# Kernel optimization log

Hardware: AMD Instinct MI355X
Metric: run time of the kernel (lower is better)

Reference implementation:

```python
import jax, jax.numpy as jnp
from jax import lax
import numpy as np

B, T, I, H, L, C = 64, 512, 128, 256, 2, 3


def _lstm_layer(x, W_ih, W_hh, b_ih, b_hh):
    # x: [B, T, in_dim]; W_ih: [4H, in_dim]; W_hh: [4H, H]
    # PyTorch gate order: i, f, g, o
    gates_x = jnp.einsum('bti,gi->btg', x, W_ih) + b_ih + b_hh  # [B, T, 4H]
    h0 = jnp.zeros((x.shape[0], W_hh.shape[1]), x.dtype)
    c0 = h0

    def step(carry, gx):
        h, c = carry
        g = gx + h @ W_hh.T  # [B, 4H]
        i, f, gg, o = jnp.split(g, 4, axis=-1)
        i = jax.nn.sigmoid(i)
        f = jax.nn.sigmoid(f)
        gg = jnp.tanh(gg)
        o = jax.nn.sigmoid(o)
        c = f * c + i * gg
        h = o * jnp.tanh(c)
        return (h, c), h

    _, hs = lax.scan(step, (h0, c0), jnp.swapaxes(gates_x, 0, 1))  # [T, B, H]
    return jnp.swapaxes(hs, 0, 1)  # [B, T, H]


def setup_inputs() -> dict:
    key = jax.random.key(0)
    ks = jax.random.split(key, 12)
    s = 1.0 / np.sqrt(H)
    u = lambda k, shape: jax.random.uniform(k, shape, jnp.float32, -s, s)
    return {
        'x': jax.random.normal(ks[0], (B, T, I), jnp.float32),
        'W_ih_0': u(ks[1], (4 * H, I)),
        'W_hh_0': u(ks[2], (4 * H, H)),
        'b_ih_0': u(ks[3], (4 * H,)),
        'b_hh_0': u(ks[4], (4 * H,)),
        'W_ih_1': u(ks[5], (4 * H, H)),
        'W_hh_1': u(ks[6], (4 * H, H)),
        'b_ih_1': u(ks[7], (4 * H,)),
        'b_hh_1': u(ks[8], (4 * H,)),
        'fc_w': u(ks[9], (C, H)),
        'fc_b': u(ks[10], (C,)),
    }


def reference(x, W_ih_0, W_hh_0, b_ih_0, b_hh_0, W_ih_1, W_hh_1, b_ih_1, b_hh_1, fc_w, fc_b):
    h = _lstm_layer(x, W_ih_0, W_hh_0, b_ih_0, b_hh_0)
    h = _lstm_layer(h, W_ih_1, W_hh_1, b_ih_1, b_hh_1)
    last = h[:, -1, :]                      # [B, H]
    logits = last @ fc_w.T + fc_b           # [B, C]
    return jax.nn.softmax(logits, axis=1)
```

## Files before the change

### kernel.cpp

```cpp
#include <hip/hip_runtime.h>
#include <cstdint>
#include <cstddef>

typedef _Float16 half2_t __attribute__((ext_vector_type(2)));
typedef _Float16 half8_t __attribute__((ext_vector_type(8)));
typedef float f32x4 __attribute__((ext_vector_type(4)));

static __device__ __forceinline__ float fdot2(half2_t a, half2_t b, float c) {
    return __builtin_amdgcn_fdot2(a, b, c, false);
}
static __device__ __forceinline__ half2_t h2(unsigned int u) {
    return __builtin_bit_cast(half2_t, u);
}
static __device__ __forceinline__ float sigm(float x) {
    return 1.f / (1.f + __expf(-x));
}
static __device__ __forceinline__ float tanh_fast(float x) {
    float ax = fabsf(x);
    float e = __expf(2.f * ax);
    float r = 1.f - 2.f / (e + 1.f);
    return copysignf(r, x);
}

__global__ __launch_bounds__(256) void prep_whh(const float* __restrict__ Whh,
                                                const float* __restrict__ bih,
                                                const float* __restrict__ bhh,
                                                uint4* __restrict__ Wp,
                                                float* __restrict__ bias) {
    int n = blockIdx.x * 256 + threadIdx.x;
    if (n < 1024) bias[n] = bih[n] + bhh[n];
    int p = n >> 9;
    int tid = n & 511;
    int g = p >> 4, u = p & 15;
    int w = tid >> 6, l = tid & 63;
    int q = l >> 5, l31 = l & 31;
    int row = g * 256 + w * 32 + l31;
    int kb = q * 128 + u * 8;
    union { uint4 u4; _Float16 h[8]; } cv;
#pragma unroll
    for (int i = 0; i < 8; ++i) cv.h[i] = (_Float16)Whh[row * 256 + kb + i];
    Wp[p * 512 + tid] = cv.u4;
}

__global__ __launch_bounds__(256) void cvt_f16(const float* __restrict__ in,
                                               _Float16* __restrict__ out, int n4) {
    int i = blockIdx.x * 256 + threadIdx.x;
    if (i < n4) {
        float4 v = ((const float4*)in)[i];
        union { ushort4 u; _Float16 h[4]; } cv;
        cv.h[0] = (_Float16)v.x; cv.h[1] = (_Float16)v.y;
        cv.h[2] = (_Float16)v.z; cv.h[3] = (_Float16)v.w;
        ((ushort4*)out)[i] = cv.u;
    }
}

__global__ __launch_bounds__(256) void gemm_mfma(const _Float16* __restrict__ A,
                                                 const _Float16* __restrict__ Bw,
                                                 const float* __restrict__ bias,
                                                 float* __restrict__ Cmat, int K) {
    __shared__ _Float16 As[64][72];
    __shared__ _Float16 Bs[64][72];
    const int tid = threadIdx.x;
    const int wave = tid >> 6, lane = tid & 63;
    const int quad = lane >> 4, l16 = lane & 15;
    const int m0 = blockIdx.x * 64, n0 = blockIdx.y * 64;
    const int sr = tid >> 2;
    const int sc = (tid & 3) * 16;

    f32x4 acc[4] = {};

    for (int k0 = 0; k0 < K; k0 += 64) {
        const uint4 a0v = *(const uint4*)(A + (size_t)(m0 + sr) * K + k0 + sc);
        const uint4 a1v = *(const uint4*)(A + (size_t)(m0 + sr) * K + k0 + sc + 8);
        const uint4 b0v = *(const uint4*)(Bw + (size_t)(n0 + sr) * K + k0 + sc);
        const uint4 b1v = *(const uint4*)(Bw + (size_t)(n0 + sr) * K + k0 + sc + 8);
        __syncthreads();
        *(uint4*)&As[sr][sc] = a0v;
        *(uint4*)&As[sr][sc + 8] = a1v;
        *(uint4*)&Bs[sr][sc] = b0v;
        *(uint4*)&Bs[sr][sc + 8] = b1v;
        __syncthreads();
#pragma unroll
        for (int kc = 0; kc < 64; kc += 32) {
            half8_t af = *(const half8_t*)&As[wave * 16 + l16][kc + quad * 8];
#pragma unroll
            for (int nb = 0; nb < 4; ++nb) {
                half8_t bf = *(const half8_t*)&Bs[nb * 16 + l16][kc + quad * 8];
                acc[nb] = __builtin_amdgcn_mfma_f32_16x16x32_f16(af, bf, acc[nb], 0, 0, 0);
            }
        }
    }
#pragma unroll
    for (int nb = 0; nb < 4; ++nb) {
#pragma unroll
        for (int i = 0; i < 4; ++i) {
            int row = m0 + wave * 16 + quad * 4 + i;
            int col = n0 + nb * 16 + l16;
            Cmat[(size_t)row * 1024 + col] = acc[nb][i] + bias[col];
        }
    }
}

__global__ __launch_bounds__(512, 2)
void lstm_scan(const float* __restrict__ gx,
               const uint4* __restrict__ Wp,
               _Float16* __restrict__ h_out,
               int store_all) {
    const int b = blockIdx.x;
    const int tid = threadIdx.x;
    const int w = tid >> 6;
    const int l = tid & 63;
    const int q = l >> 5;
    const int l31 = l & 31;
    const int j = w * 32 + l31;

    __shared__ uint4 wlds[16 * 512];
    __shared__ _Float16 hbuf[2][256] __attribute__((aligned(16)));
    __shared__ _Float16 hist[16][256] __attribute__((aligned(16)));

#pragma unroll
    for (int p = 0; p < 16; ++p) wlds[p * 512 + tid] = Wp[(48 + p) * 512 + tid];
    uint4 wreg[48];
#pragma unroll
    for (int p = 0; p < 48; ++p) wreg[p] = Wp[p * 512 + tid];

    if (tid < 256) hbuf[0][tid] = (_Float16)0.f;
    float c = 0.f;
    const float* gxb = gx + (size_t)b * 512 * 1024 + (size_t)(q * 512 + j);
    float gA = gxb[0], gB = gxb[256];
    __syncthreads();

    for (int t = 0; t < 512; ++t) {
        float gA_n = 0.f, gB_n = 0.f;
        if (t < 511) {
            gA_n = gxb[(size_t)(t + 1) * 1024];
            gB_n = gxb[(size_t)(t + 1) * 1024 + 256];
        }

        const char* hp = (const char*)&hbuf[t & 1][0] + q * 256;
        float a0 = 0.f, a1 = 0.f, a2 = 0.f, a3 = 0.f;
#pragma unroll
        for (int u = 0; u < 16; ++u) {
            const uint4 hv = *(const uint4*)(hp + u * 16);
            const uint4 w0 = wreg[u];
            const uint4 w1 = wreg[16 + u];
            const uint4 w2 = wreg[32 + u];
            const uint4 w3 = wlds[u * 512 + tid];
            a0 = fdot2(h2(w0.x), h2(hv.x), a0);
            a1 = fdot2(h2(w1.x), h2(hv.x), a1);
            a2 = fdot2(h2(w2.x), h2(hv.x), a2);
            a3 = fdot2(h2(w3.x), h2(hv.x), a3);
            a0 = fdot2(h2(w0.y), h2(hv.y), a0);
            a1 = fdot2(h2(w1.y), h2(hv.y), a1);
            a2 = fdot2(h2(w2.y), h2(hv.y), a2);
            a3 = fdot2(h2(w3.y), h2(hv.y), a3);
            a0 = fdot2(h2(w0.z), h2(hv.z), a0);
            a1 = fdot2(h2(w1.z), h2(hv.z), a1);
            a2 = fdot2(h2(w2.z), h2(hv.z), a2);
            a3 = fdot2(h2(w3.z), h2(hv.z), a3);
            a0 = fdot2(h2(w0.w), h2(hv.w), a0);
            a1 = fdot2(h2(w1.w), h2(hv.w), a1);
            a2 = fdot2(h2(w2.w), h2(hv.w), a2);
            a3 = fdot2(h2(w3.w), h2(hv.w), a3);
        }
        if (q == 0) { a0 += gA; a1 += gB; }
        else        { a2 += gA; a3 += gB; }
        a0 += __shfl_xor(a0, 32);
        a1 += __shfl_xor(a1, 32);
        a2 += __shfl_xor(a2, 32);
        a3 += __shfl_xor(a3, 32);

        const float iv = sigm(a0);
        const float fv = sigm(a1);
        const float gv = tanh_fast(a2);
        const float ov = sigm(a3);
        c = fv * c + iv * gv;
        const _Float16 hh = (_Float16)(ov * tanh_fast(c));

        if (q == 0) hbuf[(t + 1) & 1][j] = hh;
        else if (store_all) hist[t & 15][j] = hh;
        gA = gA_n; gB = gB_n;

        asm volatile("s_waitcnt lgkmcnt(0)" ::: "memory");
        __builtin_amdgcn_s_barrier();
        asm volatile("" ::: "memory");

        if (store_all && (t & 7) == 7) {
            const int s = tid >> 6, e = tid & 63;
            const int s0 = (t - 7) & 15;
            const uint2 v = *(const uint2*)&hist[s0 + s][e * 4];
            *(uint2*)(h_out + (size_t)b * 512 * 256 +
                      (size_t)(t - 7 + s) * 256 + e * 4) = v;
        }
    }
    if (!store_all && tid < 256) {
        h_out[(size_t)b * 256 + tid] = hbuf[0][tid];
    }
}

__global__ __launch_bounds__(64) void fc_softmax(const _Float16* __restrict__ hlast,
                                                 const float* __restrict__ fcw,
                                                 const float* __restrict__ fcb,
                                                 float* __restrict__ out) {
    const int b = blockIdx.x;
    const int lane = threadIdx.x;
    const _Float16* h = hlast + (size_t)b * 256;
    float p0 = 0.f, p1 = 0.f, p2 = 0.f;
    for (int k = lane; k < 256; k += 64) {
        float hv = (float)h[k];
        p0 += hv * fcw[k];
        p1 += hv * fcw[256 + k];
        p2 += hv * fcw[512 + k];
    }
#pragma unroll
    for (int off = 32; off > 0; off >>= 1) {
        p0 += __shfl_down(p0, off);
        p1 += __shfl_down(p1, off);
        p2 += __shfl_down(p2, off);
    }
    if (lane == 0) {
        float l0 = p0 + fcb[0], l1 = p1 + fcb[1], l2 = p2 + fcb[2];
        float m = fmaxf(l0, fmaxf(l1, l2));
        float e0 = __expf(l0 - m), e1 = __expf(l1 - m), e2 = __expf(l2 - m);
        float s = 1.f / (e0 + e1 + e2);
        out[b * 3 + 0] = e0 * s;
        out[b * 3 + 1] = e1 * s;
        out[b * 3 + 2] = e2 * s;
    }
}

extern "C" void kernel_launch(void* const* d_in, const int* in_sizes, int n_in,
                              void* d_out, int out_size, void* d_ws, size_t ws_size,
                              hipStream_t stream) {
    const float* x    = (const float*)d_in[0];
    const float* Wih0 = (const float*)d_in[1];
    const float* Whh0 = (const float*)d_in[2];
    const float* bih0 = (const float*)d_in[3];
    const float* bhh0 = (const float*)d_in[4];
    const float* Wih1 = (const float*)d_in[5];
    const float* Whh1 = (const float*)d_in[6];
    const float* bih1 = (const float*)d_in[7];
    const float* bhh1 = (const float*)d_in[8];
    const float* fcw  = (const float*)d_in[9];
    const float* fcb  = (const float*)d_in[10];
    float* out = (float*)d_out;

    char* ws = (char*)d_ws;
    float* gx        = (float*)ws;     ws += (size_t)32768 * 1024 * 4;
    _Float16* h0f    = (_Float16*)ws;  ws += (size_t)32768 * 256 * 2;
    _Float16* xh     = (_Float16*)ws;  ws += (size_t)32768 * 128 * 2;
    _Float16* hlast  = (_Float16*)ws;  ws += (size_t)64 * 256 * 2;
    _Float16* Wih0h  = (_Float16*)ws;  ws += (size_t)1024 * 128 * 2;
    _Float16* Wih1h  = (_Float16*)ws;  ws += (size_t)1024 * 256 * 2;
    uint4* Wp0       = (uint4*)ws;     ws += (size_t)1024 * 256 * 2;
    uint4* Wp1       = (uint4*)ws;     ws += (size_t)1024 * 256 * 2;
    float* bias0     = (float*)ws;     ws += 4096;
    float* bias1     = (float*)ws;     ws += 4096;

    prep_whh<<<128, 256, 0, stream>>>(Whh0, bih0, bhh0, Wp0, bias0);
    prep_whh<<<128, 256, 0, stream>>>(Whh1, bih1, bhh1, Wp1, bias1);
    cvt_f16<<<4096, 256, 0, stream>>>(x, xh, 32768 * 128 / 4);
    cvt_f16<<<128, 256, 0, stream>>>(Wih0, Wih0h, 1024 * 128 / 4);
    cvt_f16<<<256, 256, 0, stream>>>(Wih1, Wih1h, 1024 * 256 / 4);

    gemm_mfma<<<dim3(512, 16), 256, 0, stream>>>(xh, Wih0h, bias0, gx, 128);
    lstm_scan<<<64, 512, 0, stream>>>(gx, Wp0, h0f, 1);

    gemm_mfma<<<dim3(512, 16), 256, 0, stream>>>(h0f, Wih1h, bias1, gx, 256);
    lstm_scan<<<64, 512, 0, stream>>>(gx, Wp1, hlast, 0);

    fc_softmax<<<64, 64, 0, stream>>>(hlast, fcw, fcb, out);
}
```

Measured before the change: 1.793 ms.

## Give each LSTM scan thread a full hidden unit with more register-resident weights

The recurrent scan drops from 512 to 256 threads per block, so each thread computes the whole K=256 dot product for one hidden unit. This removes the cross-half shuffle reductions and the duplicated gate-input loads. The packed weight layout is rebuilt so 104 uint4 chunks sit in registers and 24 in LDS, with the h and LDS weight reads software-pipelined inside the loop. The trade-off is half as many waves to hide latency, twice the serial dot-product work per thread, and very high VGPR pressure that could cause spills.

```diff
diff --git a/kernel.cpp b/kernel.cpp
--- a/kernel.cpp
+++ b/kernel.cpp
@@ -29,17 +29,15 @@
                                                 float* __restrict__ bias) {
     int n = blockIdx.x * 256 + threadIdx.x;
     if (n < 1024) bias[n] = bih[n] + bhh[n];
-    int p = n >> 9;
-    int tid = n & 511;
-    int g = p >> 4, u = p & 15;
-    int w = tid >> 6, l = tid & 63;
-    int q = l >> 5, l31 = l & 31;
-    int row = g * 256 + w * 32 + l31;
-    int kb = q * 128 + u * 8;
+    int p = n >> 8;
+    int j = n & 255;
+    int g = p >> 5, u = p & 31;
+    int row = g * 256 + j;
+    int kb = u * 8;
     union { uint4 u4; _Float16 h[8]; } cv;
 #pragma unroll
     for (int i = 0; i < 8; ++i) cv.h[i] = (_Float16)Whh[row * 256 + kb + i];
-    Wp[p * 512 + tid] = cv.u4;
+    Wp[p * 256 + j] = cv.u4;
 }
 
 __global__ __launch_bounds__(256) void cvt_f16(const float* __restrict__ in,
@@ -101,51 +99,57 @@
     }
 }
 
-__global__ __launch_bounds__(512, 2)
+__global__ __launch_bounds__(256, 1)
 void lstm_scan(const float* __restrict__ gx,
                const uint4* __restrict__ Wp,
                _Float16* __restrict__ h_out,
                int store_all) {
     const int b = blockIdx.x;
-    const int tid = threadIdx.x;
-    const int w = tid >> 6;
-    const int l = tid & 63;
-    const int q = l >> 5;
-    const int l31 = l & 31;
-    const int j = w * 32 + l31;
-
-    __shared__ uint4 wlds[16 * 512];
+    const int j = threadIdx.x;
+
+    __shared__ uint4 wlds[24 * 256];
     __shared__ _Float16 hbuf[2][256] __attribute__((aligned(16)));
     __shared__ _Float16 hist[16][256] __attribute__((aligned(16)));
 
 #pragma unroll
-    for (int p = 0; p < 16; ++p) wlds[p * 512 + tid] = Wp[(48 + p) * 512 + tid];
-    uint4 wreg[48];
-#pragma unroll
-    for (int p = 0; p < 48; ++p) wreg[p] = Wp[p * 512 + tid];
-
-    if (tid < 256) hbuf[0][tid] = (_Float16)0.f;
+    for (int p = 0; p < 24; ++p) wlds[p * 256 + j] = Wp[(104 + p) * 256 + j];
+    uint4 wreg[104];
+#pragma unroll
+    for (int p = 0; p < 104; ++p) wreg[p] = Wp[p * 256 + j];
+
+    hbuf[0][j] = (_Float16)0.f;
     float c = 0.f;
-    const float* gxb = gx + (size_t)b * 512 * 1024 + (size_t)(q * 512 + j);
-    float gA = gxb[0], gB = gxb[256];
+    _Float16 last_h = (_Float16)0.f;
+    const float* gxb = gx + (size_t)b * 512 * 1024 + j;
+    float g0 = gxb[0], g1 = gxb[256], g2 = gxb[512], g3 = gxb[768];
     __syncthreads();
 
     for (int t = 0; t < 512; ++t) {
-        float gA_n = 0.f, gB_n = 0.f;
+        float n0 = 0.f, n1 = 0.f, n2 = 0.f, n3 = 0.f;
         if (t < 511) {
-            gA_n = gxb[(size_t)(t + 1) * 1024];
-            gB_n = gxb[(size_t)(t + 1) * 1024 + 256];
-        }
-
-        const char* hp = (const char*)&hbuf[t & 1][0] + q * 256;
+            const float* gxn = gxb + (size_t)(t + 1) * 1024;
+            n0 = gxn[0]; n1 = gxn[256]; n2 = gxn[512]; n3 = gxn[768];
+        }
+
+        const uint4* hb = (const uint4*)&hbuf[t & 1][0];
+        uint4 hv0 = hb[0], hv1 = hb[1];
+        uint4 ws0 = wlds[0 * 256 + j], ws1 = wlds[1 * 256 + j];
+
         float a0 = 0.f, a1 = 0.f, a2 = 0.f, a3 = 0.f;
 #pragma unroll
-        for (int u = 0; u < 16; ++u) {
-            const uint4 hv = *(const uint4*)(hp + u * 16);
+        for (int u = 0; u < 32; ++u) {
+            const uint4 hv = (u & 1) ? hv1 : hv0;
+            if (u + 2 < 32) {
+                if (u & 1) hv1 = hb[u + 2]; else hv0 = hb[u + 2];
+            }
+            const uint4 w3 = (u < 8) ? wreg[96 + u] : ((u & 1) ? ws1 : ws0);
+            if (u >= 8 && u < 30) {
+                if (u & 1) ws1 = wlds[(u - 6) * 256 + j];
+                else       ws0 = wlds[(u - 6) * 256 + j];
+            }
             const uint4 w0 = wreg[u];
-            const uint4 w1 = wreg[16 + u];
-            const uint4 w2 = wreg[32 + u];
-            const uint4 w3 = wlds[u * 512 + tid];
+            const uint4 w1 = wreg[32 + u];
+            const uint4 w2 = wreg[64 + u];
             a0 = fdot2(h2(w0.x), h2(hv.x), a0);
             a1 = fdot2(h2(w1.x), h2(hv.x), a1);
             a2 = fdot2(h2(w2.x), h2(hv.x), a2);
@@ -163,12 +167,7 @@
             a2 = fdot2(h2(w2.w), h2(hv.w), a2);
             a3 = fdot2(h2(w3.w), h2(hv.w), a3);
         }
-        if (q == 0) { a0 += gA; a1 += gB; }
-        else        { a2 += gA; a3 += gB; }
-        a0 += __shfl_xor(a0, 32);
-        a1 += __shfl_xor(a1, 32);
-        a2 += __shfl_xor(a2, 32);
-        a3 += __shfl_xor(a3, 32);
+        a0 += g0; a1 += g1; a2 += g2; a3 += g3;
 
         const float iv = sigm(a0);
         const float fv = sigm(a1);
@@ -176,25 +175,23 @@
         const float ov = sigm(a3);
         c = fv * c + iv * gv;
         const _Float16 hh = (_Float16)(ov * tanh_fast(c));
-
-        if (q == 0) hbuf[(t + 1) & 1][j] = hh;
-        else if (store_all) hist[t & 15][j] = hh;
-        gA = gA_n; gB = gB_n;
+        hbuf[(t + 1) & 1][j] = hh;
+        last_h = hh;
+        if (store_all) hist[t & 15][j] = hh;
+        g0 = n0; g1 = n1; g2 = n2; g3 = n3;
 
         asm volatile("s_waitcnt lgkmcnt(0)" ::: "memory");
         __builtin_amdgcn_s_barrier();
         asm volatile("" ::: "memory");
 
         if (store_all && (t & 7) == 7) {
-            const int s = tid >> 6, e = tid & 63;
             const int s0 = (t - 7) & 15;
-            const uint2 v = *(const uint2*)&hist[s0 + s][e * 4];
-            *(uint2*)(h_out + (size_t)b * 512 * 256 +
-                      (size_t)(t - 7 + s) * 256 + e * 4) = v;
-        }
-    }
-    if (!store_all && tid < 256) {
-        h_out[(size_t)b * 256 + tid] = hbuf[0][tid];
+            const uint4 v = *(const uint4*)((const char*)hist + s0 * 512 + j * 16);
+            *(uint4*)(h_out + (size_t)b * 512 * 256 + (size_t)(t - 7) * 256 + j * 8) = v;
+        }
+    }
+    if (!store_all) {
+        h_out[(size_t)b * 256 + j] = last_h;
     }
 }
 
@@ -264,10 +261,10 @@
     cvt_f16<<<256, 256, 0, stream>>>(Wih1, Wih1h, 1024 * 256 / 4);
 
     gemm_mfma<<<dim3(512, 16), 256, 0, stream>>>(xh, Wih0h, bias0, gx, 128);
-    lstm_scan<<<64, 512, 0, stream>>>(gx, Wp0, h0f, 1);
+    lstm_scan<<<64, 256, 0, stream>>>(gx, Wp0, h0f, 1);
 
     gemm_mfma<<<dim3(512, 16), 256, 0, stream>>>(h0f, Wih1h, bias1, gx, 256);
-    lstm_scan<<<64, 512, 0, stream>>>(gx, Wp1, hlast, 0);
+    lstm_scan<<<64, 256, 0, stream>>>(gx, Wp1, hlast, 0);
 
     fc_softmax<<<64, 64, 0, stream>>>(hlast, fcw, fcb, out);
 }
```

New measurement: 2.926 ms. 1.63x slower.
